# Kernel tuning notes

Hardware: AMD Instinct MI355X
Metric: run time of the kernel (lower is better)

The kernel has to match this reference:

```python
import jax, jax.numpy as jnp
import numpy as np


def setup_inputs() -> dict:
    key = jax.random.key(0)
    ks = jax.random.split(key, 8)
    B, S, Nc, C, Cseed = 4, 4096, 8192, 512, 256
    return {
        "query_xyz": jax.random.normal(ks[0], (B, S, 3), dtype=jnp.float32),
        "ref_xyz": jax.random.normal(ks[1], (B, Nc, 3), dtype=jnp.float32),
        "ref_feat": jax.random.normal(ks[2], (B, C, Nc), dtype=jnp.float32),
        "seed_features": jax.random.normal(ks[3], (B, Cseed, S), dtype=jnp.float32),
        "W_seed_proj": jax.random.normal(ks[4], (Cseed, C), dtype=jnp.float32) * 0.02,
        "b_seed_proj": jax.random.normal(ks[5], (Cseed,), dtype=jnp.float32) * 0.02,
        "W_concat_proj": jax.random.normal(ks[6], (Cseed, 2 * Cseed), dtype=jnp.float32) * 0.02,
        "b_concat_proj": jax.random.normal(ks[7], (Cseed,), dtype=jnp.float32) * 0.02,
    }


def _nn_gather(query_xyz, ref_xyz, ref_feat):
    # torch.cdist(p=2) + argmin: argmin over squared distance is identical
    # (sqrt is monotonic), so we skip the sqrt.
    q2 = jnp.sum(query_xyz * query_xyz, axis=-1, keepdims=True)      # (B,S,1)
    r2 = jnp.sum(ref_xyz * ref_xyz, axis=-1)[:, None, :]             # (B,1,Nc)
    qr = jnp.einsum("bsd,bnd->bsn", query_xyz, ref_xyz)              # (B,S,Nc)
    d2 = q2 + r2 - 2.0 * qr                                          # (B,S,Nc)
    idx = jnp.argmin(d2, axis=-1)                                    # (B,S) int
    # gather nearest-neighbor features: (B,C,Nc) -> (B,C,S)
    return jnp.take_along_axis(ref_feat, idx[:, None, :], axis=2)


def reference(query_xyz, ref_xyz, ref_feat, seed_features,
              W_seed_proj, b_seed_proj, W_concat_proj, b_concat_proj):
    lift3d_raw = _nn_gather(query_xyz, ref_xyz, ref_feat)            # (B,C,S)
    # 1x1 Conv1d == channel matmul
    lift3d_seed = jnp.einsum("oc,bcs->bos", W_seed_proj, lift3d_raw) \
                  + b_seed_proj[None, :, None]                       # (B,256,S)
    fused = jnp.concatenate([seed_features, lift3d_seed], axis=1)    # (B,512,S)
    out = jnp.einsum("oc,bcs->bos", W_concat_proj, fused) \
          + b_concat_proj[None, :, None]                             # (B,256,S)
    return out
```

## Files before the change

### kernel.cpp

```cpp
#include <hip/hip_runtime.h>

#define B_   4
#define S_   4096
#define NC   8192
#define C_   512
#define CS   256
#define KTOT 768

typedef __attribute__((ext_vector_type(8))) short short8;
typedef __attribute__((ext_vector_type(4))) float f32x4;

static __device__ __forceinline__ unsigned short f2bf(float x) {
    unsigned u = __builtin_bit_cast(unsigned, x);
    unsigned r = u + 0x7FFFu + ((u >> 16) & 1u);
    return (unsigned short)(r >> 16);
}

__global__ __launch_bounds__(256) void prep_kernel(
        const float* __restrict__ rxyz, float4* __restrict__ refpk,
        const float* __restrict__ Wcat, const float* __restrict__ Wseed,
        unsigned short* __restrict__ Wcomb,
        const float* __restrict__ bseed, const float* __restrict__ bcat,
        float* __restrict__ beff) {
    __shared__ float sa[64][68];
    __shared__ float sbt[64][68];
    int bid = blockIdx.x;
    int tid = threadIdx.x;

    if (bid < 64) {
        int w = tid >> 6, l = tid & 63;
        int o = bid * 4 + w;
        float4 wv = *(const float4*)(Wcat + (size_t)o * 512 + 256 + l * 4);
        float4 bb = *(const float4*)(bseed + l * 4);
        float acc = __fmul_rn(wv.x, bb.x);
        acc = fmaf(wv.y, bb.y, acc);
        acc = fmaf(wv.z, bb.z, acc);
        acc = fmaf(wv.w, bb.w, acc);
        #pragma unroll
        for (int off = 32; off > 0; off >>= 1) acc += __shfl_down(acc, off);
        if (l == 0) beff[o] = acc + bcat[o];
    } else if (bid < 96) {
        int xb = bid - 64;
        int tc = (xb & 7) * 64;
        int to = (xb >> 3) * 64;
        int tx = tid & 15, ty = tid >> 4;
        float acc[4][4] = {};
        for (int kt = 0; kt < 256; kt += 64) {
            __syncthreads();
            #pragma unroll
            for (int r = 0; r < 4; ++r) {
                int oo = r * 16 + ty;
                float4 v = *(const float4*)(Wcat + (size_t)(to + oo) * 512 + 256 + kt + tx * 4);
                sa[oo][tx * 4 + 0] = v.x;
                sa[oo][tx * 4 + 1] = v.y;
                sa[oo][tx * 4 + 2] = v.z;
                sa[oo][tx * 4 + 3] = v.w;
                float4 u = *(const float4*)(Wseed + (size_t)(kt + oo) * 512 + tc + tx * 4);
                sbt[oo][tx * 4 + 0] = u.x;
                sbt[oo][tx * 4 + 1] = u.y;
                sbt[oo][tx * 4 + 2] = u.z;
                sbt[oo][tx * 4 + 3] = u.w;
            }
            __syncthreads();
            for (int k = 0; k < 64; ++k) {
                float a[4], bb2[4];
                #pragma unroll
                for (int i = 0; i < 4; ++i) a[i] = sa[ty * 4 + i][k];
                #pragma unroll
                for (int j = 0; j < 4; ++j) bb2[j] = sbt[k][tx * 4 + j];
                #pragma unroll
                for (int i = 0; i < 4; ++i)
                    #pragma unroll
                    for (int j = 0; j < 4; ++j)
                        acc[i][j] = fmaf(a[i], bb2[j], acc[i][j]);
            }
        }
        #pragma unroll
        for (int i = 0; i < 4; ++i)
            #pragma unroll
            for (int j = 0; j < 4; ++j)
                Wcomb[(size_t)(to + ty * 4 + i) * KTOT + 256 + tc + tx * 4 + j] = f2bf(acc[i][j]);
    } else if (bid < 160) {
        int g = ((bid - 96) * 256 + tid) * 4;
        int o = g >> 8, cc = g & 255;
        float4 v = *(const float4*)(Wcat + (size_t)o * 512 + cc);
        ushort4 ov;
        ov.x = f2bf(v.x); ov.y = f2bf(v.y); ov.z = f2bf(v.z); ov.w = f2bf(v.w);
        *(ushort4*)(Wcomb + (size_t)o * KTOT + cc) = ov;
    } else {
        int gid = (bid - 160) * 256 + tid;
        float x = rxyz[gid * 3 + 0];
        float y = rxyz[gid * 3 + 1];
        float z = rxyz[gid * 3 + 2];
        float r2 = __fadd_rn(__fadd_rn(__fmul_rn(x, x), __fmul_rn(y, y)), __fmul_rn(z, z));
        refpk[gid] = make_float4(x, y, z, r2);
    }
}

__global__ __launch_bounds__(256, 4) void mid_kernel(
        const float* __restrict__ qxyz, const float4* __restrict__ refpk,
        float* __restrict__ pval, int* __restrict__ pidx,
        const float* __restrict__ rf, unsigned short* __restrict__ refT,
        const float* __restrict__ seed, unsigned short* __restrict__ seedT) {
    __shared__ float t[64][65];
    int bid = blockIdx.x;
    int tid = threadIdx.x;
    int r7 = bid % 7;
    int g7 = bid / 7;

    if (r7 == 0 || r7 == 4) {
        int aid = g7 * 2 + (r7 == 4);
        int sblk = aid & 127;
        int c = (aid >> 7) & 3;
        int b = aid >> 9;
        int lane = tid & 63;
        int qg = tid >> 6;
        int sbase = sblk * 32 + qg * 8;

        float qx[8], qy[8], qz[8], q2[8];
        #pragma unroll
        for (int q = 0; q < 8; ++q) {
            const float* qp = qxyz + ((size_t)(b * S_ + sbase + q)) * 3;
            qx[q] = qp[0]; qy[q] = qp[1]; qz[q] = qp[2];
            q2[q] = __fadd_rn(__fadd_rn(__fmul_rn(qx[q], qx[q]), __fmul_rn(qy[q], qy[q])),
                              __fmul_rn(qz[q], qz[q]));
        }

        const float4* ep = refpk + (size_t)b * NC + c * 2048 + lane;
        float best[8];
        int bj[8];
        #pragma unroll
        for (int q = 0; q < 8; ++q) { best[q] = 3.4028235e38f; bj[q] = 0; }

        float4 r0 = ep[0];
        float4 r1 = ep[64];
        #pragma unroll 2
        for (int j = 0; j < 32; j += 2) {
            float4 r2 = r0, r3 = r1;
            if (j + 2 < 32) {
                r2 = ep[(j + 2) * 64];
                r3 = ep[(j + 3) * 64];
            }
            #pragma unroll
            for (int q = 0; q < 8; ++q) {
                float qr = __fadd_rn(__fadd_rn(__fmul_rn(qx[q], r0.x), __fmul_rn(qy[q], r0.y)),
                                     __fmul_rn(qz[q], r0.z));
                float s = __fadd_rn(q2[q], r0.w);
                float d2 = fmaf(qr, -2.0f, s);
                if (d2 < best[q]) { best[q] = d2; bj[q] = j; }
            }
            #pragma unroll
            for (int q = 0; q < 8; ++q) {
                float qr = __fadd_rn(__fadd_rn(__fmul_rn(qx[q], r1.x), __fmul_rn(qy[q], r1.y)),
                                     __fmul_rn(qz[q], r1.z));
                float s = __fadd_rn(q2[q], r1.w);
                float d2 = fmaf(qr, -2.0f, s);
                if (d2 < best[q]) { best[q] = d2; bj[q] = j + 1; }
            }
            r0 = r2;
            r1 = r3;
        }

        int bx[8];
        #pragma unroll
        for (int q = 0; q < 8; ++q) bx[q] = c * 2048 + bj[q] * 64 + lane;

        #pragma unroll
        for (int m = 1; m < 64; m <<= 1) {
            #pragma unroll
            for (int q = 0; q < 8; ++q) {
                float vv = __shfl_xor(best[q], m, 64);
                int xx = __shfl_xor(bx[q], m, 64);
                if (vv < best[q] || (vv == best[q] && xx < bx[q])) {
                    best[q] = vv; bx[q] = xx;
                }
            }
        }
        if (lane == 0) {
            #pragma unroll
            for (int q = 0; q < 8; ++q) {
                int qs = b * S_ + sbase + q;
                pval[qs * 4 + c] = best[q];
                pidx[qs * 4 + c] = bx[q];
            }
        }
    } else if (r7 != 6) {
        int id = g7 * 4 + (r7 - 1 - (r7 > 4 ? 1 : 0));
        int b = id >> 10;
        int c0 = ((id >> 7) & 7) * 64;
        int n0 = (id & 127) * 64;
        int tx = tid & 15, ty = tid >> 4;
        #pragma unroll
        for (int r = 0; r < 4; ++r) {
            int cc = r * 16 + ty;
            float4 v = *(const float4*)(rf + ((size_t)b * C_ + c0 + cc) * NC + n0 + tx * 4);
            t[tx * 4 + 0][cc] = v.x;
            t[tx * 4 + 1][cc] = v.y;
            t[tx * 4 + 2][cc] = v.z;
            t[tx * 4 + 3][cc] = v.w;
        }
        __syncthreads();
        #pragma unroll
        for (int r = 0; r < 4; ++r) {
            int n = r * 16 + ty;
            ushort4 o;
            o.x = f2bf(t[n][tx * 4 + 0]);
            o.y = f2bf(t[n][tx * 4 + 1]);
            o.z = f2bf(t[n][tx * 4 + 2]);
            o.w = f2bf(t[n][tx * 4 + 3]);
            *(ushort4*)(refT + ((size_t)b * NC + n0 + n) * C_ + c0 + tx * 4) = o;
        }
    } else {
        int id = g7;
        int b = id >> 8;
        int rem = id & 255;
        int c0 = (rem >> 6) * 64;
        int s0 = (rem & 63) * 64;
        int tx = tid & 15, ty = tid >> 4;
        #pragma unroll
        for (int r = 0; r < 4; ++r) {
            int cc = r * 16 + ty;
            float4 v = *(const float4*)(seed + ((size_t)b * CS + c0 + cc) * S_ + s0 + tx * 4);
            t[tx * 4 + 0][cc] = v.x;
            t[tx * 4 + 1][cc] = v.y;
            t[tx * 4 + 2][cc] = v.z;
            t[tx * 4 + 3][cc] = v.w;
        }
        __syncthreads();
        #pragma unroll
        for (int r = 0; r < 4; ++r) {
            int n = r * 16 + ty;
            ushort4 o;
            o.x = f2bf(t[n][tx * 4 + 0]);
            o.y = f2bf(t[n][tx * 4 + 1]);
            o.z = f2bf(t[n][tx * 4 + 2]);
            o.w = f2bf(t[n][tx * 4 + 3]);
            *(ushort4*)(seedT + ((size_t)b * S_ + s0 + n) * CS + c0 + tx * 4) = o;
        }
    }
}

__global__ __launch_bounds__(256) void fused_gemm_kernel(
        const unsigned short* __restrict__ Wcomb,
        const unsigned short* __restrict__ seedT,
        const unsigned short* __restrict__ refT,
        const float* __restrict__ pval,
        const int* __restrict__ pidx,
        const float* __restrict__ beff,
        float* __restrict__ out) {
    __shared__ __align__(16) unsigned short sA[2][64][72];
    __shared__ __align__(16) unsigned short sB[2][128][72];
    __shared__ int sIdx[128];
    __shared__ float sBias[64];

    int tid = threadIdx.x;
    int b = blockIdx.z;
    int m0 = blockIdx.y * 64;
    int s0 = blockIdx.x * 128;
    if (tid < 128) {
        int qs = b * S_ + s0 + tid;
        float v = pval[qs * 4 + 0];
        int x = pidx[qs * 4 + 0];
        #pragma unroll
        for (int c = 1; c < 4; ++c) {
            float vv = pval[qs * 4 + c];
            int xx = pidx[qs * 4 + c];
            if (vv < v || (vv == v && xx < x)) { v = vv; x = xx; }
        }
        sIdx[tid] = x & (NC - 1);
        if (tid < 64) sBias[tid] = beff[m0 + tid];
    }

    int lane = tid & 63;
    int w = tid >> 6;
    int wm = w >> 1;
    int wn = w & 1;
    int ln = lane & 15;
    int quad = lane >> 4;
    int q8 = quad * 8;

    int mmA  = tid >> 2;
    int kk16 = (tid & 3) << 4;
    int nB   = tid >> 1;
    int kk32 = (tid & 1) << 5;
    const unsigned short* Arow = Wcomb + (size_t)(m0 + mmA) * KTOT + kk16;
    const unsigned short* Srow = seedT + ((size_t)b * S_ + s0 + nB) * CS + kk32;

    f32x4 acc[2][4];
    #pragma unroll
    for (int i = 0; i < 2; ++i)
        #pragma unroll
        for (int j = 0; j < 4; ++j)
            acc[i][j] = (f32x4){0.f, 0.f, 0.f, 0.f};

    short8 ra0, ra1, rb0, rb1, rb2, rb3;

    #define SLOAD(PK) do {                                                         \
        int pk0 = (PK) * 64;                                                       \
        ra0 = *(const short8*)(Arow + pk0);                                        \
        ra1 = *(const short8*)(Arow + pk0 + 8);                                    \
        const unsigned short* Brow =                                               \
            (pk0 < 256) ? (Srow + pk0)                                             \
                        : (refT + ((size_t)b * NC + sIdx[nB]) * C_                 \
                           + (pk0 - 256) + kk32);                                  \
        rb0 = *(const short8*)(Brow);                                              \
        rb1 = *(const short8*)(Brow + 8);                                          \
        rb2 = *(const short8*)(Brow + 16);                                         \
        rb3 = *(const short8*)(Brow + 24);                                         \
    } while (0)

    #define SWRITE(BUF) do {                                                       \
        *(short8*)&sA[BUF][mmA][kk16]      = ra0;                                  \
        *(short8*)&sA[BUF][mmA][kk16 + 8]  = ra1;                                  \
        *(short8*)&sB[BUF][nB][kk32]       = rb0;                                  \
        *(short8*)&sB[BUF][nB][kk32 + 8]   = rb1;                                  \
        *(short8*)&sB[BUF][nB][kk32 + 16]  = rb2;                                  \
        *(short8*)&sB[BUF][nB][kk32 + 24]  = rb3;                                  \
    } while (0)

    SLOAD(0);
    SWRITE(0);
    __syncthreads();

    int cur = 0;
    for (int ks = 0; ks < 12; ++ks) {
        if (ks < 11) SLOAD(ks + 1);
        #pragma unroll
        for (int kf = 0; kf < 2; ++kf) {
            short8 af[2], bfr[4];
            #pragma unroll
            for (int i = 0; i < 2; ++i)
                af[i] = *(const short8*)&sA[cur][wm * 32 + i * 16 + ln][kf * 32 + q8];
            #pragma unroll
            for (int j = 0; j < 4; ++j)
                bfr[j] = *(const short8*)&sB[cur][wn * 64 + j * 16 + ln][kf * 32 + q8];
            #pragma unroll
            for (int i = 0; i < 2; ++i)
                #pragma unroll
                for (int j = 0; j < 4; ++j)
                    acc[i][j] = __builtin_amdgcn_mfma_f32_16x16x32_bf16(af[i], bfr[j], acc[i][j], 0, 0, 0);
        }
        if (ks < 11) {
            SWRITE(cur ^ 1);
            __syncthreads();
            cur ^= 1;
        }
    }
    #undef SLOAD
    #undef SWRITE

    #pragma unroll
    for (int i = 0; i < 2; ++i) {
        int mb = wm * 32 + i * 16 + quad * 4;
        #pragma unroll
        for (int j = 0; j < 4; ++j) {
            int col = s0 + wn * 64 + j * 16 + ln;
            #pragma unroll
            for (int r = 0; r < 4; ++r) {
                int m = mb + r;
                out[((size_t)b * CS + m0 + m) * S_ + col] = acc[i][j][r] + sBias[m];
            }
        }
    }
}

extern "C" void kernel_launch(void* const* d_in, const int* in_sizes, int n_in,
                              void* d_out, int out_size, void* d_ws, size_t ws_size,
                              hipStream_t stream) {
    const float* qxyz  = (const float*)d_in[0];
    const float* rxyz  = (const float*)d_in[1];
    const float* rfeat = (const float*)d_in[2];
    const float* seed  = (const float*)d_in[3];
    const float* Wseed = (const float*)d_in[4];
    const float* bseed = (const float*)d_in[5];
    const float* Wcat  = (const float*)d_in[6];
    const float* bcat  = (const float*)d_in[7];
    float* out = (float*)d_out;

    char* ws = (char*)d_ws;
    float* pval           = (float*)(ws);
    int* pidx             = (int*)(ws + 262144);
    float* beff           = (float*)(ws + 524288);
    float4* refpk         = (float4*)(ws + 528384);
    unsigned short* Wcomb = (unsigned short*)(ws + 1052672);
    unsigned short* refT  = (unsigned short*)(ws + 1445888);
    unsigned short* seedT = (unsigned short*)(ws + 35000320);

    hipLaunchKernelGGL(prep_kernel, dim3(288), dim3(256), 0, stream,
                       rxyz, refpk, Wcat, Wseed, Wcomb, bseed, bcat, beff);
    hipLaunchKernelGGL(mid_kernel, dim3(7168), dim3(256), 0, stream,
                       qxyz, refpk, pval, pidx, rfeat, refT, seed, seedT);
    hipLaunchKernelGGL(fused_gemm_kernel, dim3(32, 4, 4), dim3(256), 0, stream,
                       Wcomb, seedT, refT, pval, pidx, beff, out);
}
```

Measured before the change: 182.6 us.

## Load GEMM fragments directly from global memory, dropping LDS double buffering

The fused GEMM kernel no longer stages A and B tiles through double-buffered shared memory. Each wave now loads its MFMA operand fragments straight from global memory (weights, transposed seed features, gathered ref features) inside a fully unrolled K loop. This removes LDS writes and reads and the per-step barriers, and frees shared memory for occupancy. In exchange, fragments shared by several waves are fetched repeatedly through cache, and the explicit prefetch overlap is lost.

```diff
diff --git a/kernel.cpp b/kernel.cpp
--- a/kernel.cpp
+++ b/kernel.cpp
@@ -248,8 +248,6 @@
         const int* __restrict__ pidx,
         const float* __restrict__ beff,
         float* __restrict__ out) {
-    __shared__ __align__(16) unsigned short sA[2][64][72];
-    __shared__ __align__(16) unsigned short sB[2][128][72];
     __shared__ int sIdx[128];
     __shared__ float sBias[64];
 
@@ -270,6 +268,7 @@
         sIdx[tid] = x & (NC - 1);
         if (tid < 64) sBias[tid] = beff[m0 + tid];
     }
+    __syncthreads();
 
     int lane = tid & 63;
     int w = tid >> 6;
@@ -279,12 +278,18 @@
     int quad = lane >> 4;
     int q8 = quad * 8;
 
-    int mmA  = tid >> 2;
-    int kk16 = (tid & 3) << 4;
-    int nB   = tid >> 1;
-    int kk32 = (tid & 1) << 5;
-    const unsigned short* Arow = Wcomb + (size_t)(m0 + mmA) * KTOT + kk16;
-    const unsigned short* Srow = seedT + ((size_t)b * S_ + s0 + nB) * CS + kk32;
+    const unsigned short* Abase[2];
+    #pragma unroll
+    for (int i = 0; i < 2; ++i)
+        Abase[i] = Wcomb + (size_t)(m0 + wm * 32 + i * 16 + ln) * KTOT + q8;
+    const unsigned short* Sbase[4];
+    const unsigned short* Gbase[4];
+    #pragma unroll
+    for (int j = 0; j < 4; ++j) {
+        int row = wn * 64 + j * 16 + ln;
+        Sbase[j] = seedT + ((size_t)b * S_ + s0 + row) * CS + q8;
+        Gbase[j] = refT + ((size_t)b * NC + sIdx[row]) * C_ + q8;
+    }
 
     f32x4 acc[2][4];
     #pragma unroll
@@ -293,61 +298,31 @@
         for (int j = 0; j < 4; ++j)
             acc[i][j] = (f32x4){0.f, 0.f, 0.f, 0.f};
 
-    short8 ra0, ra1, rb0, rb1, rb2, rb3;
-
-    #define SLOAD(PK) do {                                                         \
-        int pk0 = (PK) * 64;                                                       \
-        ra0 = *(const short8*)(Arow + pk0);                                        \
-        ra1 = *(const short8*)(Arow + pk0 + 8);                                    \
-        const unsigned short* Brow =                                               \
-            (pk0 < 256) ? (Srow + pk0)                                             \
-                        : (refT + ((size_t)b * NC + sIdx[nB]) * C_                 \
-                           + (pk0 - 256) + kk32);                                  \
-        rb0 = *(const short8*)(Brow);                                              \
-        rb1 = *(const short8*)(Brow + 8);                                          \
-        rb2 = *(const short8*)(Brow + 16);                                         \
-        rb3 = *(const short8*)(Brow + 24);                                         \
-    } while (0)
-
-    #define SWRITE(BUF) do {                                                       \
-        *(short8*)&sA[BUF][mmA][kk16]      = ra0;                                  \
-        *(short8*)&sA[BUF][mmA][kk16 + 8]  = ra1;                                  \
-        *(short8*)&sB[BUF][nB][kk32]       = rb0;                                  \
-        *(short8*)&sB[BUF][nB][kk32 + 8]   = rb1;                                  \
-        *(short8*)&sB[BUF][nB][kk32 + 16]  = rb2;                                  \
-        *(short8*)&sB[BUF][nB][kk32 + 24]  = rb3;                                  \
-    } while (0)
-
-    SLOAD(0);
-    SWRITE(0);
-    __syncthreads();
-
-    int cur = 0;
+    #pragma unroll
     for (int ks = 0; ks < 12; ++ks) {
-        if (ks < 11) SLOAD(ks + 1);
         #pragma unroll
         for (int kf = 0; kf < 2; ++kf) {
+            int k = ks * 64 + kf * 32;
             short8 af[2], bfr[4];
             #pragma unroll
             for (int i = 0; i < 2; ++i)
-                af[i] = *(const short8*)&sA[cur][wm * 32 + i * 16 + ln][kf * 32 + q8];
-            #pragma unroll
-            for (int j = 0; j < 4; ++j)
-                bfr[j] = *(const short8*)&sB[cur][wn * 64 + j * 16 + ln][kf * 32 + q8];
+                af[i] = *(const short8*)(Abase[i] + k);
+            if (k < 256) {
+                #pragma unroll
+                for (int j = 0; j < 4; ++j)
+                    bfr[j] = *(const short8*)(Sbase[j] + k);
+            } else {
+                #pragma unroll
+                for (int j = 0; j < 4; ++j)
+                    bfr[j] = *(const short8*)(Gbase[j] + (k - 256));
+            }
             #pragma unroll
             for (int i = 0; i < 2; ++i)
                 #pragma unroll
                 for (int j = 0; j < 4; ++j)
                     acc[i][j] = __builtin_amdgcn_mfma_f32_16x16x32_bf16(af[i], bfr[j], acc[i][j], 0, 0, 0);
         }
-        if (ks < 11) {
-            SWRITE(cur ^ 1);
-            __syncthreads();
-            cur ^= 1;
-        }
-    }
-    #undef SLOAD
-    #undef SWRITE
+    }
 
     #pragma unroll
     for (int i = 0; i < 2; ++i) {
```

New measurement: 201.3 us. 10.2% more time.
